# Optimization experiments

Measured on AMD Instinct MI355X. Metric: run time of the kernel, lower is better.

Reference implementation:

```python
import jax, jax.numpy as jnp
import numpy as np

DECAY = 0.99
EPS = 1e-5
BETA = 0.25

def _l2norm(v, axis=-1):
    # F.normalize: x / max(||x||, 1e-12)
    n = jnp.sqrt(jnp.sum(v * v, axis=axis, keepdims=True))
    return v / jnp.maximum(n, 1e-12)

def setup_inputs() -> dict:
    key = jax.random.key(0)
    k0, k1, k2, k3 = jax.random.split(key, 4)
    B, C, H, W, E, K = 8, 256, 64, 64, 32, 8192
    x = jax.random.normal(k0, (B, C, H, W), jnp.float32)
    Wq = jax.random.normal(k1, (E, C), jnp.float32) * 0.05  # 1x1 conv kernel
    bq = jnp.zeros((E,), jnp.float32)
    emb = jax.random.normal(k2, (K, E), jnp.float32)
    emb = _l2norm(emb, axis=1)  # matches F.normalize init in __init__
    ema_cluster_size = jnp.ones((K,), jnp.float32)
    ema_weight = emb  # consistent post-init EMA state
    return {"x": x, "Wq": Wq, "bq": bq, "embedding": emb,
            "ema_cluster_size": ema_cluster_size, "ema_weight": ema_weight}

def reference(x, Wq, bq, embedding, ema_cluster_size, ema_weight):
    B, C, H, W = x.shape
    E = Wq.shape[0]
    K = embedding.shape[0]
    # quant_conv: 1x1 conv == per-pixel linear
    z = jnp.einsum('bchw,ec->behw', x, Wq) + bq[None, :, None, None]  # [B,E,H,W]
    z_flat = z.transpose(0, 2, 3, 1).reshape(-1, E)  # [N,E]
    # get_idx(use_znorm=True): cosine similarity argmax (== argmin L2 on normalized)
    zn = _l2norm(z_flat, axis=1)
    en = _l2norm(embedding, axis=1)
    indices = jnp.argmax(zn @ en.T, axis=1)  # [N]
    # codebook gather (raw embedding, as in torch)
    z_q = embedding[indices].reshape(B, H, W, E).transpose(0, 3, 1, 2)  # [B,E,H,W]
    # EMA update (training path; scatter == one-hot.T @ z_flat / one-hot.sum)
    counts = jax.ops.segment_sum(jnp.ones((z_flat.shape[0],), z_flat.dtype), indices, num_segments=K)
    dw = jax.ops.segment_sum(z_flat, indices, num_segments=K)  # [K,E]
    new_cs = DECAY * ema_cluster_size + (1.0 - DECAY) * counts
    new_w = DECAY * ema_weight + (1.0 - DECAY) * dw
    n = jnp.sum(new_cs)
    cs_smoothed = (new_cs + EPS) / (n + K * EPS) * n
    new_embedding = new_w / cs_smoothed[:, None]
    # commitment loss + straight-through
    qloss = BETA * jnp.mean((jax.lax.stop_gradient(z_q) - z) ** 2)
    z_q_st = z + jax.lax.stop_gradient(z_q - z)
    return (z_q_st, indices.reshape(B, H, W), qloss, new_embedding, new_cs, new_w)
```

## Files before the change

### kernel.cpp

```cpp
#include <hip/hip_runtime.h>

#define B_ 8
#define C_ 256
#define HW_ 4096
#define E_ 32
#define K_ 8192
#define N_ 32768
#define NCHUNK 4
#define KC_ (K_ / NCHUNK)
#define NSTAGE (KC_ / 128)
#define KSEG 32

#define DECAY_ 0.99f
#define OMD_   0.01f
#define EPS_   1e-5f
#define BETA_  0.25f

#define O_ZQ   0
#define O_IDX  1048576
#define O_QL   1081344
#define O_NEMB 1081345
#define O_NCS  1343489
#define O_NW   1351681

#define WS_EH   0u
#define WS_EM   131072u
#define WS_Z    262144u
#define WS_PACK 1310720u
#define WS_PCS  1572864u
#define WS_QP   1572992u

typedef float f32x4 __attribute__((ext_vector_type(4)));
typedef short s16x8 __attribute__((ext_vector_type(8)));
typedef unsigned long long u64;

__device__ __forceinline__ unsigned short f2bf(float f) {
    unsigned u = __float_as_uint(f);
    u = u + 0x7fffu + ((u >> 16) & 1u);
    return (unsigned short)(u >> 16);
}
__device__ __forceinline__ float bf2f(unsigned short h) {
    return __uint_as_float(((unsigned)h) << 16);
}
__device__ __forceinline__ unsigned ford(float f) {
    unsigned u = __float_as_uint(f);
    return (u & 0x80000000u) ? ~u : (u | 0x80000000u);
}
__device__ __forceinline__ int imax(int a, int b) { return a > b ? a : b; }
__device__ __forceinline__ int imin(int a, int b) { return a < b ? a : b; }

__device__ __forceinline__ void gload_lds16(const void* g, void* l) {
    __builtin_amdgcn_global_load_lds(
        (const __attribute__((address_space(1))) unsigned int*)g,
        (__attribute__((address_space(3))) unsigned int*)l, 16, 0, 0);
}

__global__ __launch_bounds__(256) void k_pre(const float* __restrict__ emb,
                                             const float* __restrict__ cs,
                                             uint4* __restrict__ eh16,
                                             uint4* __restrict__ em16,
                                             float* __restrict__ part_cs,
                                             const float* __restrict__ x,
                                             const float* __restrict__ Wq,
                                             const float* __restrict__ bq,
                                             float* __restrict__ zout) {
    __shared__ float wqt[C_ * E_];
    int tid = threadIdx.x;

    if (blockIdx.x < 128) {
        int t4 = blockIdx.x * 256 + tid;
        int k = t4 >> 2, q = t4 & 3;
        const float4* r = (const float4*)(emb + (size_t)k * E_ + q * 8);
        float4 u0 = r[0], u1 = r[1];
        float ss = u0.x*u0.x + u0.y*u0.y + u0.z*u0.z + u0.w*u0.w
                 + u1.x*u1.x + u1.y*u1.y + u1.z*u1.z + u1.w*u1.w;
        ss += __shfl_xor(ss, 1, 64);
        ss += __shfl_xor(ss, 2, 64);
        float inv = 1.0f / fmaxf(sqrtf(ss), 1e-12f);

        float v[8] = {u0.x, u0.y, u0.z, u0.w, u1.x, u1.y, u1.z, u1.w};
        unsigned short h1a[8], h2a[8];
#pragma unroll
        for (int e = 0; e < 8; e++) {
            float en = v[e] * inv;
            unsigned short h1 = f2bf(en);
            float r1 = en - bf2f(h1);
            h1a[e] = h1; h2a[e] = f2bf(r1);
        }
        int t = k >> 4, c15 = k & 15;
        eh16[t * 64 + q * 16 + c15] = ((uint4*)h1a)[0];
        em16[t * 64 + q * 16 + c15] = ((uint4*)h2a)[0];

        if (tid < 64) {
            float cv = cs[blockIdx.x * 64 + tid];
#pragma unroll
            for (int off = 32; off > 0; off >>= 1) cv += __shfl_down(cv, off);
            if (tid == 0) part_cs[blockIdx.x] = cv;
        }
        return;
    }

    int zb = blockIdx.x - 128;
#pragma unroll
    for (int i = 0; i < 32; i++) {
        int g = i * 256 + tid;
        int e = g >> 8;
        int c = g & 255;
        wqt[c * E_ + e] = Wq[g];
    }
    __syncthreads();
    int lp = tid & 63, eg = tid >> 6;
    int n0 = zb * 64 + lp;
    int b  = n0 >> 12, hw = n0 & (HW_ - 1);
    const float* xp = x + (size_t)b * C_ * HW_ + hw;
    float a[8];
#pragma unroll
    for (int j = 0; j < 8; j++) a[j] = 0.f;
#pragma unroll 4
    for (int c = 0; c < C_; c++) {
        float xv = xp[(size_t)c * HW_];
        const float4* wr = (const float4*)(wqt + c * E_ + eg * 8);
        float4 w0 = wr[0], w1 = wr[1];
        a[0] += xv * w0.x; a[1] += xv * w0.y; a[2] += xv * w0.z; a[3] += xv * w0.w;
        a[4] += xv * w1.x; a[5] += xv * w1.y; a[6] += xv * w1.z; a[7] += xv * w1.w;
    }
    float4 o0 = make_float4(a[0] + bq[eg*8+0], a[1] + bq[eg*8+1],
                            a[2] + bq[eg*8+2], a[3] + bq[eg*8+3]);
    float4 o1 = make_float4(a[4] + bq[eg*8+4], a[5] + bq[eg*8+5],
                            a[6] + bq[eg*8+6], a[7] + bq[eg*8+7]);
    float4* zg = (float4*)(zout + (size_t)n0 * E_ + eg * 8);
    zg[0] = o0; zg[1] = o1;
}

__global__ __launch_bounds__(256, 4) void k_score_mfma(const float* __restrict__ zws,
                                                       const char* __restrict__ ehb,
                                                       const char* __restrict__ emb_b,
                                                       int2* __restrict__ pk2) {
    __shared__ __align__(16) char smem[32768];

    int tid  = threadIdx.x;
    int lane = tid & 63;
    int w    = tid >> 6;
    int chunk = blockIdx.y;

    s16x8 a1, a2;
    {
        int ploc = w * 16 + (lane & 15);
        int n0   = blockIdx.x * 64 + ploc;
        int e0   = (lane >> 4) * 8;
        const float4* zp = (const float4*)(zws + (size_t)n0 * E_ + e0);
        float4 z0 = zp[0], z1 = zp[1];
        float zz[8] = {z0.x, z0.y, z0.z, z0.w, z1.x, z1.y, z1.z, z1.w};
#pragma unroll
        for (int j = 0; j < 8; j++) {
            float zv = zz[j] * 134217728.0f;
            unsigned short h1 = f2bf(zv);
            float r1 = zv - bf2f(h1);
            a1[j] = (short)h1; a2[j] = (short)f2bf(r1);
        }
    }

    const char* srcp[4];
#pragma unroll
    for (int i = 0; i < 4; i++) {
        int d = i * 256 + tid;
        int pl = d >> 9, dd = d & 511;
        srcp[i] = (pl ? emb_b : ehb) + (size_t)chunk * (KC_ * 64) + dd * 16;
    }

#pragma unroll
    for (int i = 0; i < 4; i++)
        gload_lds16(srcp[i], smem + (i * 256 + tid) * 16);
    __syncthreads();

    int rbase = 8191 - chunk * KC_ - (lane & 15);
    int bq1[4], bq2[4];
#pragma unroll
    for (int j = 0; j < 4; j++) { bq1[j] = (int)0x80000000; bq2[j] = (int)0x80000000; }
    f32x4 zero4 = {0.f, 0.f, 0.f, 0.f};

    for (int st = 0; st < NSTAGE; st++) {
        if (st + 1 < NSTAGE) {
            char* dst = smem + ((st + 1) & 1) * 16384;
#pragma unroll
            for (int i = 0; i < 4; i++)
                gload_lds16(srcp[i] + (size_t)(st + 1) * 8192, dst + (i * 256 + tid) * 16);
        }
        const char* cur = smem + (st & 1) * 16384;
        int rst = rbase - st * 128;

#pragma unroll
        for (int g = 0; g < 2; g++) {
            int ct = g * 4;
            s16x8 b1[4], b2[4];
#pragma unroll
            for (int q = 0; q < 4; q++) {
                b1[q] = ((const s16x8*)(cur +        (ct + q) * 1024))[lane];
                b2[q] = ((const s16x8*)(cur + 8192 + (ct + q) * 1024))[lane];
            }
            f32x4 acc[4];
#pragma unroll
            for (int q = 0; q < 4; q++)
                acc[q] = __builtin_amdgcn_mfma_f32_16x16x32_bf16(a1, b1[q], zero4, 0, 0, 0);
#pragma unroll
            for (int q = 0; q < 4; q++)
                acc[q] = __builtin_amdgcn_mfma_f32_16x16x32_bf16(a1, b2[q], acc[q], 0, 0, 0);
#pragma unroll
            for (int q = 0; q < 4; q++)
                acc[q] = __builtin_amdgcn_mfma_f32_16x16x32_bf16(a2, b1[q], acc[q], 0, 0, 0);
            int r0 = rst - ct * 16;
#pragma unroll
            for (int j = 0; j < 4; j++) {
                int v0 = ((int)acc[0][j] & (int)0xFFFFE000) | r0;
                int v1 = ((int)acc[1][j] & (int)0xFFFFE000) | (r0 - 16);
                int v2 = ((int)acc[2][j] & (int)0xFFFFE000) | (r0 - 32);
                int v3 = ((int)acc[3][j] & (int)0xFFFFE000) | (r0 - 48);
                int hi = imax(imax(v0, v1), imax(v2, v3));
                int m  = imin(bq1[j], hi);
                bq1[j] = imax(bq1[j], hi);
                bq2[j] = imax(bq2[j], m);
            }
        }
        __syncthreads();
    }

#pragma unroll
    for (int off = 1; off < 16; off <<= 1) {
#pragma unroll
        for (int j = 0; j < 4; j++) {
            int o1 = __shfl_xor(bq1[j], off, 64);
            int o2 = __shfl_xor(bq2[j], off, 64);
            int m  = imin(bq1[j], o1);
            bq1[j] = imax(bq1[j], o1);
            bq2[j] = imax(imax(bq2[j], o2), m);
        }
    }
    if ((lane & 15) == 0) {
        int rowbase = blockIdx.x * 64 + w * 16 + (lane >> 4) * 4;
#pragma unroll
        for (int j = 0; j < 4; j++)
            pk2[(size_t)chunk * N_ + rowbase + j] = make_int2(bq1[j], bq2[j]);
    }
}

__device__ __forceinline__ float rescore(const float* __restrict__ emb, int k,
                                         const float* zrow) {
    const float4* r = (const float4*)(emb + (size_t)k * E_);
    float4 v[8];
    float ss = 0.f;
#pragma unroll
    for (int i = 0; i < 8; i++) {
        v[i] = r[i];
        ss += v[i].x * v[i].x + v[i].y * v[i].y + v[i].z * v[i].z + v[i].w * v[i].w;
    }
    float inv = 1.0f / fmaxf(sqrtf(ss), 1e-12f);
    const float4* zp = (const float4*)zrow;
    float sx = 0.f, sy = 0.f, sz = 0.f, sw = 0.f;
#pragma unroll
    for (int i = 0; i < 8; i++) {
        float4 e4 = make_float4(v[i].x * inv, v[i].y * inv, v[i].z * inv, v[i].w * inv);
        float4 zr = zp[i];
        sx += zr.x * e4.x; sy += zr.y * e4.y;
        sz += zr.z * e4.z; sw += zr.w * e4.w;
    }
    return (sx + sy) + (sz + sw);
}

__global__ __launch_bounds__(256) void k_scatter(const float* __restrict__ zws,
                                                 const int2* __restrict__ pk2,
                                                 const float* __restrict__ emb,
                                                 float* __restrict__ out_zq,
                                                 float* __restrict__ out_idx,
                                                 float* __restrict__ qpart) {
    __shared__ float zbuf[64 * E_];
    __shared__ int   idxs_s[64];
    __shared__ float red[4];
    int tid = threadIdx.x;

    const float4* zsrc = (const float4*)(zws + (size_t)blockIdx.x * 64 * E_);
    float4* zdst = (float4*)zbuf;
    zdst[tid]       = zsrc[tid];
    zdst[tid + 256] = zsrc[tid + 256];
    __syncthreads();

    {
        int p = tid >> 2, c4 = tid & 3;
        int nn = blockIdx.x * 64 + p;
        int2 c2 = pk2[(size_t)c4 * N_ + nn];
        u64 pkd = 0;
#pragma unroll
        for (int t = 0; t < 2; t++) {
            int raw = t ? c2.y : c2.x;
            int k = 8191 - (raw & 0x1fff);
            k = k < 0 ? 0 : (k > K_ - 1 ? K_ - 1 : k);
            float s = rescore(emb, k, zbuf + p * E_);
            u64 pk = ((u64)ford(s) << 32) | (unsigned)(K_ - 1 - k);
            pkd = pkd > pk ? pkd : pk;
        }
        u64 o = __shfl_xor(pkd, 1, 64); pkd = pkd > o ? pkd : o;
        o = __shfl_xor(pkd, 2, 64);     pkd = pkd > o ? pkd : o;
        if (c4 == 0) {
            int bi = K_ - 1 - (int)(unsigned)(pkd & 0xffffffffu);
            idxs_s[p] = bi;
            out_idx[nn] = (float)bi;
        }
    }
    __syncthreads();

    int lp = tid & 63, eg = tid >> 6;
    int n  = blockIdx.x * 64 + lp;
    int b  = n >> 12, hw = n & (HW_ - 1);
    int idx = idxs_s[lp];
    const float* er = emb + (size_t)idx * E_ + eg * 8;
    float* o = out_zq + (size_t)b * E_ * HW_ + (size_t)(eg * 8) * HW_ + hw;

    float sq = 0.f;
#pragma unroll
    for (int j = 0; j < 8; j++) {
        float zv = zbuf[lp * E_ + eg * 8 + j];
        float qf = er[j];
        float d = qf - zv;
        sq += d * d;
        o[(size_t)j * HW_] = qf;
    }

#pragma unroll
    for (int off = 32; off > 0; off >>= 1) sq += __shfl_down(sq, off);
    int lane = tid & 63, wid = tid >> 6;
    if (lane == 0) red[wid] = sq;
    __syncthreads();
    if (tid == 0) qpart[blockIdx.x] = red[0] + red[1] + red[2] + red[3];
}

__global__ __launch_bounds__(256) void k_dwfinal(const float* __restrict__ zws,
                                                 const float* __restrict__ idxf,
                                                 const float* __restrict__ cs,
                                                 const float* __restrict__ ew,
                                                 const float* __restrict__ part_cs,
                                                 const float* __restrict__ qpart,
                                                 float* __restrict__ out_nw,
                                                 float* __restrict__ out_nemb,
                                                 float* __restrict__ out_ncs,
                                                 float* __restrict__ out_ql) {
    __shared__ float acc[KSEG * E_];
    __shared__ int   cnt_s[KSEG];
    __shared__ float nsum_s;
    int tid = threadIdx.x;
    int kbase = blockIdx.x * KSEG;

#pragma unroll
    for (int i = 0; i < KSEG * E_ / 256; i++) acc[tid + i * 256] = 0.f;
    if (tid < KSEG) cnt_s[tid] = 0;
    __syncthreads();

    const float4* idx4 = (const float4*)idxf;
#pragma unroll 2
    for (int it = 0; it < N_ / 1024; ++it) {
        float4 f = idx4[it * 256 + tid];
        int n0 = (it * 256 + tid) * 4;
        int ii[4] = {(int)f.x, (int)f.y, (int)f.z, (int)f.w};
#pragma unroll
        for (int s = 0; s < 4; s++) {
            unsigned d = (unsigned)(ii[s] - kbase);
            if (d < (unsigned)KSEG) {
                const float4* zr = (const float4*)(zws + (size_t)(n0 + s) * E_);
                float* ap = acc + d * E_;
#pragma unroll
                for (int j = 0; j < 8; j++) {
                    float4 v = zr[j];
                    atomicAdd(ap + j * 4 + 0, v.x);
                    atomicAdd(ap + j * 4 + 1, v.y);
                    atomicAdd(ap + j * 4 + 2, v.z);
                    atomicAdd(ap + j * 4 + 3, v.w);
                }
                atomicAdd(cnt_s + d, 1);
            }
        }
    }

    if (tid < 64) {
        float s = part_cs[tid] + part_cs[tid + 64];
#pragma unroll
        for (int off = 32; off > 0; off >>= 1) s += __shfl_down(s, off);
        if (tid == 0) nsum_s = DECAY_ * s + OMD_ * (float)N_;
    }
    __syncthreads();
    float nsum = nsum_s;

#pragma unroll
    for (int i = 0; i < 4; i++) {
        int local = tid + i * 256;
        int kl = local >> 5, c = local & 31;
        int k = kbase + kl;
        float v = DECAY_ * ew[(size_t)k * E_ + c] + OMD_ * acc[local];
        out_nw[(size_t)k * E_ + c] = v;
        float csk = DECAY_ * cs[k] + OMD_ * (float)cnt_s[kl];
        float denom = (csk + EPS_) / (nsum + (float)K_ * EPS_) * nsum;
        out_nemb[(size_t)k * E_ + c] = v / denom;
        if (c == 0) out_ncs[k] = csk;
    }

    if (blockIdx.x == 0 && tid < 64) {
        float s = 0.f;
#pragma unroll
        for (int i = 0; i < 8; i++) s += qpart[tid + i * 64];
#pragma unroll
        for (int off = 32; off > 0; off >>= 1) s += __shfl_down(s, off);
        if (tid == 0) out_ql[0] = BETA_ * s / (float)(B_ * E_ * HW_);
    }
}

extern "C" void kernel_launch(void* const* d_in, const int* in_sizes, int n_in,
                              void* d_out, int out_size, void* d_ws, size_t ws_size,
                              hipStream_t stream) {
    const float* x   = (const float*)d_in[0];
    const float* Wq  = (const float*)d_in[1];
    const float* bq  = (const float*)d_in[2];
    const float* emb = (const float*)d_in[3];
    const float* cs  = (const float*)d_in[4];
    const float* ew  = (const float*)d_in[5];
    float* out = (float*)d_out;
    float* ws  = (float*)d_ws;

    k_pre<<<128 + N_ / 64, 256, 0, stream>>>(emb, cs,
        (uint4*)(ws + WS_EH), (uint4*)(ws + WS_EM), ws + WS_PCS,
        x, Wq, bq, ws + WS_Z);
    k_score_mfma<<<dim3(N_ / 64, NCHUNK), 256, 0, stream>>>(ws + WS_Z,
        (const char*)(ws + WS_EH), (const char*)(ws + WS_EM),
        (int2*)(ws + WS_PACK));
    k_scatter<<<N_ / 64, 256, 0, stream>>>(ws + WS_Z,
        (const int2*)(ws + WS_PACK), emb,
        out + O_ZQ, out + O_IDX, ws + WS_QP);
    k_dwfinal<<<K_ / KSEG, 256, 0, stream>>>(ws + WS_Z, out + O_IDX, cs, ew,
                                             ws + WS_PCS, ws + WS_QP,
                                             out + O_NW, out + O_NEMB,
                                             out + O_NCS, out + O_QL);
}
```

Measured before the change: 207.6 us.

## Widen score blocks to 128 pixels and wave-cooperative EMA scatter

The scoring kernel now runs 512-thread blocks covering 128 pixels each, so every codebook stage staged in shared memory is reused by twice as many pixels and global codebook traffic is halved. In the EMA accumulation kernel, each wave uses ballot and shuffle to find the pixels that fall in its codebook segment, then loads and atomically adds each matching z row cooperatively across 32 lanes instead of one thread doing 32 scalar atomics. This aims to cut redundant codebook loads and serialized per-thread atomics. The trade-offs are fewer blocks per SM for the larger score kernel and a serial per-hit loop within each wave.

```diff
diff --git a/kernel.cpp b/kernel.cpp
--- a/kernel.cpp
+++ b/kernel.cpp
@@ -10,6 +10,7 @@
 #define KC_ (K_ / NCHUNK)
 #define NSTAGE (KC_ / 128)
 #define KSEG 32
+#define PIX 128
 
 #define DECAY_ 0.99f
 #define OMD_   0.01f
@@ -132,10 +133,10 @@
     zg[0] = o0; zg[1] = o1;
 }
 
-__global__ __launch_bounds__(256, 4) void k_score_mfma(const float* __restrict__ zws,
-                                                       const char* __restrict__ ehb,
-                                                       const char* __restrict__ emb_b,
-                                                       int2* __restrict__ pk2) {
+__global__ __launch_bounds__(512) void k_score_mfma(const float* __restrict__ zws,
+                                                    const char* __restrict__ ehb,
+                                                    const char* __restrict__ emb_b,
+                                                    int2* __restrict__ pk2) {
     __shared__ __align__(16) char smem[32768];
 
     int tid  = threadIdx.x;
@@ -146,7 +147,7 @@
     s16x8 a1, a2;
     {
         int ploc = w * 16 + (lane & 15);
-        int n0   = blockIdx.x * 64 + ploc;
+        int n0   = blockIdx.x * PIX + ploc;
         int e0   = (lane >> 4) * 8;
         const float4* zp = (const float4*)(zws + (size_t)n0 * E_ + e0);
         float4 z0 = zp[0], z1 = zp[1];
@@ -160,17 +161,17 @@
         }
     }
 
-    const char* srcp[4];
-#pragma unroll
-    for (int i = 0; i < 4; i++) {
-        int d = i * 256 + tid;
+    const char* srcp[2];
+#pragma unroll
+    for (int i = 0; i < 2; i++) {
+        int d = i * 512 + tid;
         int pl = d >> 9, dd = d & 511;
         srcp[i] = (pl ? emb_b : ehb) + (size_t)chunk * (KC_ * 64) + dd * 16;
     }
 
 #pragma unroll
-    for (int i = 0; i < 4; i++)
-        gload_lds16(srcp[i], smem + (i * 256 + tid) * 16);
+    for (int i = 0; i < 2; i++)
+        gload_lds16(srcp[i], smem + (i * 512 + tid) * 16);
     __syncthreads();
 
     int rbase = 8191 - chunk * KC_ - (lane & 15);
@@ -183,8 +184,8 @@
         if (st + 1 < NSTAGE) {
             char* dst = smem + ((st + 1) & 1) * 16384;
 #pragma unroll
-            for (int i = 0; i < 4; i++)
-                gload_lds16(srcp[i] + (size_t)(st + 1) * 8192, dst + (i * 256 + tid) * 16);
+            for (int i = 0; i < 2; i++)
+                gload_lds16(srcp[i] + (size_t)(st + 1) * 8192, dst + (i * 512 + tid) * 16);
         }
         const char* cur = smem + (st & 1) * 16384;
         int rst = rbase - st * 128;
@@ -236,7 +237,7 @@
         }
     }
     if ((lane & 15) == 0) {
-        int rowbase = blockIdx.x * 64 + w * 16 + (lane >> 4) * 4;
+        int rowbase = blockIdx.x * PIX + w * 16 + (lane >> 4) * 4;
 #pragma unroll
         for (int j = 0; j < 4; j++)
             pk2[(size_t)chunk * N_ + rowbase + j] = make_int2(bq1[j], bq2[j]);
@@ -346,6 +347,8 @@
     __shared__ int   cnt_s[KSEG];
     __shared__ float nsum_s;
     int tid = threadIdx.x;
+    int lane = tid & 63;
+    int w    = tid >> 6;
     int kbase = blockIdx.x * KSEG;
 
 #pragma unroll
@@ -353,30 +356,26 @@
     if (tid < KSEG) cnt_s[tid] = 0;
     __syncthreads();
 
-    const float4* idx4 = (const float4*)idxf;
-#pragma unroll 2
-    for (int it = 0; it < N_ / 1024; ++it) {
-        float4 f = idx4[it * 256 + tid];
-        int n0 = (it * 256 + tid) * 4;
-        int ii[4] = {(int)f.x, (int)f.y, (int)f.z, (int)f.w};
-#pragma unroll
-        for (int s = 0; s < 4; s++) {
-            unsigned d = (unsigned)(ii[s] - kbase);
-            if (d < (unsigned)KSEG) {
-                const float4* zr = (const float4*)(zws + (size_t)(n0 + s) * E_);
-                float* ap = acc + d * E_;
-#pragma unroll
-                for (int j = 0; j < 8; j++) {
-                    float4 v = zr[j];
-                    atomicAdd(ap + j * 4 + 0, v.x);
-                    atomicAdd(ap + j * 4 + 1, v.y);
-                    atomicAdd(ap + j * 4 + 2, v.z);
-                    atomicAdd(ap + j * 4 + 3, v.w);
-                }
-                atomicAdd(cnt_s + d, 1);
+    int base = w * (N_ / 4);
+    for (int it = 0; it < (N_ / 4) / 64; ++it) {
+        int nbase = base + it * 64;
+        int ii = (int)idxf[nbase + lane];
+        unsigned d = (unsigned)(ii - kbase);
+        u64 m = __ballot(d < (unsigned)KSEG);
+        while (m) {
+            int src = (int)__builtin_ctzll(m);
+            m &= m - 1;
+            int dl = __shfl((int)d, src, 64);
+            int nn = nbase + src;
+            if (lane < E_) {
+                float zv = zws[(size_t)nn * E_ + lane];
+                atomicAdd(acc + dl * E_ + lane, zv);
+            } else if (lane == E_) {
+                atomicAdd(cnt_s + dl, 1);
             }
         }
     }
+    __syncthreads();
 
     if (tid < 64) {
         float s = part_cs[tid] + part_cs[tid + 64];
@@ -425,7 +424,7 @@
     k_pre<<<128 + N_ / 64, 256, 0, stream>>>(emb, cs,
         (uint4*)(ws + WS_EH), (uint4*)(ws + WS_EM), ws + WS_PCS,
         x, Wq, bq, ws + WS_Z);
-    k_score_mfma<<<dim3(N_ / 64, NCHUNK), 256, 0, stream>>>(ws + WS_Z,
+    k_score_mfma<<<dim3(N_ / PIX, NCHUNK), 512, 0, stream>>>(ws + WS_Z,
         (const char*)(ws + WS_EH), (const char*)(ws + WS_EM),
         (int2*)(ws + WS_PACK));
     k_scatter<<<N_ / 64, 256, 0, stream>>>(ws + WS_Z,
```

Measured after the change: 210.9 us. About the same (+1.6%).
